# Optimization experiments

Hardware: AMD Instinct MI355X
Metric: run time of the kernel (lower is better)

## Reference

```python
import jax, jax.numpy as jnp
import numpy as np

B, C, H, W = 8, 512, 64, 64
K = 8  # shrink factor: qk channels = C//K, v channels = C//2


def conv1x1(x, w, b):
    # x: [B,C_in,H,W], w: [C_out,C_in], b: [C_out]  (1x1 conv == channel matmul)
    return jnp.einsum('bchw,oc->bohw', x, w) + b[None, :, None, None]


def maxpool2x2(x):
    b, c, h, w = x.shape
    return x.reshape(b, c, h // 2, 2, w // 2, 2).max(axis=(3, 5))


def setup_inputs() -> dict:
    key = jax.random.key(0)
    ks = jax.random.split(key, 9)
    Cqk, Cv = C // K, C // 2
    sc = lambda fan_in: 1.0 / np.sqrt(fan_in)
    return {
        'x': jax.random.normal(ks[0], (B, C, H, W), jnp.float32),
        'Wf': jax.random.normal(ks[1], (Cqk, C), jnp.float32) * sc(C),
        'bf': jnp.zeros((Cqk,), jnp.float32),
        'Wg': jax.random.normal(ks[2], (Cqk, C), jnp.float32) * sc(C),
        'bg': jnp.zeros((Cqk,), jnp.float32),
        'Wh': jax.random.normal(ks[3], (Cv, C), jnp.float32) * sc(C),
        'bh': jnp.zeros((Cv,), jnp.float32),
        'Wv': jax.random.normal(ks[4], (C, Cv), jnp.float32) * sc(Cv),
        'bv': jnp.zeros((C,), jnp.float32),
        'gamma': jnp.float32(0.5),
    }


def reference(x, Wf, bf, Wg, bg, Wh, bh, Wv, bv, gamma):
    b, c, h, w = x.shape
    f = conv1x1(x, Wf, bf).reshape(b, c // K, h * w)          # [B, C/K, HW]
    g = maxpool2x2(conv1x1(x, Wg, bg))                         # [B, C/K, H/2, W/2]
    v = maxpool2x2(conv1x1(x, Wh, bh))                         # [B, C/2, H/2, W/2]
    hwp = (h // 2) * (w // 2)
    g = g.reshape(b, c // K, hwp)
    v = v.reshape(b, c // 2, hwp)
    # s[b, n, m] = sum_c f[b,c,n] g[b,c,m]; softmax over m (no scaling, per SAGAN)
    s = jnp.einsum('bcn,bcm->bnm', f, g)                       # [B, HW, HW']
    beta = jax.nn.softmax(s, axis=-1)
    o = jnp.einsum('bcm,bnm->bcn', v, beta).reshape(b, c // 2, h, w)
    return gamma * conv1x1(o, Wv, bv) + x
```

## Files before the change

kernel.cpp:

```cpp
#include <hip/hip_runtime.h>
#include <cstddef>

typedef __attribute__((ext_vector_type(4))) float f32x4;
typedef __attribute__((ext_vector_type(16))) float f32x16;
typedef __attribute__((ext_vector_type(8))) short bf16x8;

#define MFMA16(A, B, C) __builtin_amdgcn_mfma_f32_16x16x32_bf16(A, B, C, 0, 0, 0)
#define MFMA32(A, B, C) __builtin_amdgcn_mfma_f32_32x32x16_bf16(A, B, C, 0, 0, 0)
#define AS1 __attribute__((address_space(1)))
#define AS3 __attribute__((address_space(3)))

__device__ __forceinline__ unsigned short f2bf(float f) {
  unsigned u = __float_as_uint(f);
  u += 0x7fffu + ((u >> 16) & 1u);
  return (unsigned short)(u >> 16);
}
__device__ __forceinline__ float bf2f(unsigned short s) {
  return __uint_as_float(((unsigned)s) << 16);
}

__device__ __forceinline__ void cvt_split8(float4 a, float4 b, bf16x8* H, bf16x8* L) {
  float v[8] = {a.x, a.y, a.z, a.w, b.x, b.y, b.z, b.w};
  unsigned hh[4], ll[4];
  #pragma unroll
  for (int p = 0; p < 4; ++p) {
    unsigned short h0 = f2bf(v[2 * p]), h1 = f2bf(v[2 * p + 1]);
    hh[p] = (unsigned)h0 | ((unsigned)h1 << 16);
    unsigned short l0 = f2bf(v[2 * p] - bf2f(h0));
    unsigned short l1 = f2bf(v[2 * p + 1] - bf2f(h1));
    ll[p] = (unsigned)l0 | ((unsigned)l1 << 16);
  }
  uint4 uh; uh.x = hh[0]; uh.y = hh[1]; uh.z = hh[2]; uh.w = hh[3];
  uint4 ul; ul.x = ll[0]; ul.y = ll[1]; ul.z = ll[2]; ul.w = ll[3];
  *H = *(bf16x8*)&uh;
  *L = *(bf16x8*)&ul;
}

__device__ __forceinline__ bf16x8 cvt_hi8(float4 a, float4 b) {
  float v[8] = {a.x, a.y, a.z, a.w, b.x, b.y, b.z, b.w};
  unsigned hh[4];
  #pragma unroll
  for (int p = 0; p < 4; ++p)
    hh[p] = (unsigned)f2bf(v[2 * p]) | ((unsigned)f2bf(v[2 * p + 1]) << 16);
  uint4 uh; uh.x = hh[0]; uh.y = hh[1]; uh.z = hh[2]; uh.w = hh[3];
  return *(bf16x8*)&uh;
}


__global__ void prep_k(const float* __restrict__ Wf, const float* __restrict__ Wg,
                       const float* __restrict__ Wh, const float* __restrict__ Wv,
                       unsigned short* __restrict__ wfh, unsigned short* __restrict__ wfl,
                       unsigned short* __restrict__ wgh, unsigned short* __restrict__ wgl,
                       unsigned short* __restrict__ whb, unsigned short* __restrict__ wvb) {
  int i = blockIdx.x * 256 + threadIdx.x;
  if (i < 65536) {
    int ii = i & 32767;
    int j = ii & 7, slot = (ii >> 3) & 63, q = slot & 15, qt2 = slot >> 4;
    int kt = (ii >> 9) & 15, oct = ii >> 13;
    const float* src = (i < 32768) ? Wf : Wg;
    unsigned short* dh = (i < 32768) ? wfh : wgh;
    unsigned short* dl = (i < 32768) ? wfl : wgl;
    float v = src[(oct * 16 + q) * 512 + kt * 32 + qt2 * 8 + j];
    unsigned short h = f2bf(v);
    dh[ii] = h; dl[ii] = f2bf(v - bf2f(h));
  } else if (i < 196608) {
    int ii = i - 65536;
    int j = ii & 7, slot = (ii >> 3) & 63, q = slot & 15, qt2 = slot >> 4;
    int kt = (ii >> 9) & 15, oct = ii >> 13;
    whb[ii] = f2bf(Wh[(oct * 16 + q) * 512 + kt * 32 + qt2 * 8 + j]);
  } else if (i < 327680) {
    int ii = i - 196608;
    int j = ii & 7, slot = (ii >> 3) & 63, q = slot & 15, qt2 = slot >> 4;
    int kt = (ii >> 9) & 7, oct = ii >> 12;
    wvb[ii] = f2bf(Wv[(oct * 16 + q) * 256 + kt * 32 + qt2 * 8 + j]);
  }
}


#define STAGEX(XP, CN) { _Pragma("unroll") \
  for (int c_ = 0; c_ < 4; ++c_) \
    __builtin_amdgcn_global_load_lds( \
      (const AS1 unsigned int*)(xg + (size_t)((CN) * 32 + c_ * 2) * 4096), \
      (AS3 unsigned int*)((XP) + (w * 8 + c_ * 2) * 128), 16, 0, 0); }

#define STAGEW0(WP, CN) { \
  const unsigned short* Wt_ = (w == 0) ? wfh_ : (w == 1) ? wfl_ : (w == 2) ? wgh_ : wgl_; \
  _Pragma("unroll") \
  for (int ot_ = 0; ot_ < 4; ++ot_) \
    __builtin_amdgcn_global_load_lds( \
      (const AS1 unsigned int*)(Wt_ + (((size_t)(ot_ * 16 + (CN))) << 9) + lane * 8), \
      (AS3 unsigned int*)((WP) + (w * 4 + ot_) * 512), 16, 0, 0); }

#define STAGEW1(WP, CN) { _Pragma("unroll") \
  for (int i_ = 0; i_ < 4; ++i_) \
    __builtin_amdgcn_global_load_lds( \
      (const AS1 unsigned int*)(whb_ + (((size_t)((w * 4 + i_) * 16 + (CN))) << 9) + lane * 8), \
      (AS3 unsigned int*)((WP) + (w * 4 + i_) * 512), 16, 0, 0); }

__global__ __launch_bounds__(256, 2)
void conv_all(const float* __restrict__ x,
              const unsigned short* __restrict__ wfh_, const unsigned short* __restrict__ wfl_,
              const unsigned short* __restrict__ wgh_, const unsigned short* __restrict__ wgl_,
              const unsigned short* __restrict__ whb_,
              const float* __restrict__ bf_, const float* __restrict__ bg_,
              const float* __restrict__ bh_,
              unsigned short* __restrict__ fhi, unsigned short* __restrict__ flo,
              unsigned short* __restrict__ ghi, unsigned short* __restrict__ glo,
              unsigned short* __restrict__ vp)
{
  __shared__ __align__(16) char smem[65536];
  float* xs0 = (float*)smem;
  float* xs1 = (float*)(smem + 16384);
  unsigned short* ws0 = (unsigned short*)(smem + 32768);
  unsigned short* ws1 = (unsigned short*)(smem + 49152);
  const int bid = blockIdx.x;
  const int b = bid & 7;
  const int idx = bid >> 3;
  const int role = idx & 1;
  const int hp = idx >> 1;
  const int n0 = hp * 128;
  const int tid = threadIdx.x, w = tid >> 6, lane = tid & 63, q = lane & 15, qt = lane >> 4;
  const float* xg = x + ((size_t)(b * 512 + w * 8 + (lane >> 5)) * 4096) + n0 + (lane & 31) * 4;

  if (role == 0) {
    f32x4 accf[2][4], accg[2][4];
    #pragma unroll
    for (int nt = 0; nt < 2; ++nt)
      #pragma unroll
      for (int ot = 0; ot < 4; ++ot) {
        accf[nt][ot] = (f32x4){0.f, 0.f, 0.f, 0.f};
        accg[nt][ot] = (f32x4){0.f, 0.f, 0.f, 0.f};
      }
    STAGEX(xs0, 0) STAGEW0(ws0, 0)
    __syncthreads();
    for (int cc = 0; cc < 16; ++cc) {
      const float* xsp = (cc & 1) ? xs1 : xs0;
      const unsigned short* wp = (cc & 1) ? ws1 : ws0;
      float* xsn = (cc & 1) ? xs0 : xs1;
      unsigned short* wn = (cc & 1) ? ws0 : ws1;
      if (cc < 15) { STAGEX(xsn, cc + 1) STAGEW0(wn, cc + 1) }
      bf16x8 Ah[2], Al[2];
      #pragma unroll
      for (int nt = 0; nt < 2; ++nt) {
        const int row = w * 32 + nt * 16 + q;
        float xv[8];
        #pragma unroll
        for (int j = 0; j < 8; ++j)
          xv[j] = xsp[(qt * 8 + j) * 128 + row];
        float4 a0; a0.x = xv[0]; a0.y = xv[1]; a0.z = xv[2]; a0.w = xv[3];
        float4 a1; a1.x = xv[4]; a1.y = xv[5]; a1.z = xv[6]; a1.w = xv[7];
        cvt_split8(a0, a1, &Ah[nt], &Al[nt]);
      }
      {
        bf16x8 Bh[4], Bl[4];
        #pragma unroll
        for (int ot = 0; ot < 4; ++ot) {
          Bh[ot] = *(const bf16x8*)&wp[(0 + ot) * 512 + lane * 8];
          Bl[ot] = *(const bf16x8*)&wp[(4 + ot) * 512 + lane * 8];
        }
        #pragma unroll
        for (int nt = 0; nt < 2; ++nt)
          #pragma unroll
          for (int ot = 0; ot < 4; ++ot) {
            accf[nt][ot] = MFMA16(Ah[nt], Bh[ot], accf[nt][ot]);
            accf[nt][ot] = MFMA16(Ah[nt], Bl[ot], accf[nt][ot]);
            accf[nt][ot] = MFMA16(Al[nt], Bh[ot], accf[nt][ot]);
          }
      }
      {
        bf16x8 Bh[4], Bl[4];
        #pragma unroll
        for (int ot = 0; ot < 4; ++ot) {
          Bh[ot] = *(const bf16x8*)&wp[(8 + ot) * 512 + lane * 8];
          Bl[ot] = *(const bf16x8*)&wp[(12 + ot) * 512 + lane * 8];
        }
        #pragma unroll
        for (int nt = 0; nt < 2; ++nt)
          #pragma unroll
          for (int ot = 0; ot < 4; ++ot) {
            accg[nt][ot] = MFMA16(Ah[nt], Bh[ot], accg[nt][ot]);
            accg[nt][ot] = MFMA16(Ah[nt], Bl[ot], accg[nt][ot]);
            accg[nt][ot] = MFMA16(Al[nt], Bh[ot], accg[nt][ot]);
          }
      }
      __syncthreads();
    }
    #pragma unroll
    for (int nt = 0; nt < 2; ++nt)
      #pragma unroll
      for (int ot = 0; ot < 4; ++ot)
        #pragma unroll
        for (int r = 0; r < 4; ++r) {
          float v = accf[nt][ot][r] + bf_[ot * 16 + q];
          unsigned short h = f2bf(v);
          size_t o = (((size_t)(b * 128 + hp * 4 + w) * 4 + ot) * 64 +
                      (q >> 3) * 32 + nt * 16 + qt * 4 + r) * 8 + (q & 7);
          fhi[o] = h;
          flo[o] = f2bf(v - bf2f(h));
        }
    float (*pl)[67] = (float(*)[67])smem;
    #pragma unroll
    for (int nt = 0; nt < 2; ++nt)
      #pragma unroll
      for (int ot = 0; ot < 4; ++ot)
        #pragma unroll
        for (int r = 0; r < 4; ++r)
          pl[w * 32 + nt * 16 + qt * 4 + r][ot * 16 + q] = accg[nt][ot][r];
    __syncthreads();
    const int c = tid & 63;
    #pragma unroll
    for (int it = 0; it < 8; ++it) {
      int wp2 = (tid >> 6) + it * 4;
      float v = fmaxf(fmaxf(pl[2 * wp2][c], pl[2 * wp2 + 1][c]),
                      fmaxf(pl[64 + 2 * wp2][c], pl[65 + 2 * wp2][c])) + bg_[c];
      unsigned short h = f2bf(v);
      size_t o = (((size_t)(b * 32 + hp) * 4 + (c >> 4)) * 64 +
                  ((c >> 3) & 1) * 32 + wp2) * 8 + (c & 7);
      ghi[o] = h;
      glo[o] = f2bf(v - bf2f(h));
    }
  } else {
    f32x4 acc[2][16];
    #pragma unroll
    for (int nt = 0; nt < 2; ++nt)
      #pragma unroll
      for (int ot = 0; ot < 16; ++ot) acc[nt][ot] = (f32x4){0.f, 0.f, 0.f, 0.f};
    STAGEX(xs0, 0) STAGEW1(ws0, 0)
    __syncthreads();
    for (int cc = 0; cc < 16; ++cc) {
      const float* xsp = (cc & 1) ? xs1 : xs0;
      const unsigned short* wp = (cc & 1) ? ws1 : ws0;
      float* xsn = (cc & 1) ? xs0 : xs1;
      unsigned short* wn = (cc & 1) ? ws0 : ws1;
      if (cc < 15) { STAGEX(xsn, cc + 1) STAGEW1(wn, cc + 1) }
      bf16x8 A_[2];
      #pragma unroll
      for (int nt = 0; nt < 2; ++nt) {
        const int row = w * 32 + nt * 16 + q;
        float xv[8];
        #pragma unroll
        for (int j = 0; j < 8; ++j)
          xv[j] = xsp[(qt * 8 + j) * 128 + row];
        float4 a0; a0.x = xv[0]; a0.y = xv[1]; a0.z = xv[2]; a0.w = xv[3];
        float4 a1; a1.x = xv[4]; a1.y = xv[5]; a1.z = xv[6]; a1.w = xv[7];
        A_[nt] = cvt_hi8(a0, a1);
      }
      #pragma unroll
      for (int oh = 0; oh < 2; ++oh) {
        bf16x8 B_[8];
        #pragma unroll
        for (int ot = 0; ot < 8; ++ot)
          B_[ot] = *(const bf16x8*)&wp[(oh * 8 + ot) * 512 + lane * 8];
        #pragma unroll
        for (int nt = 0; nt < 2; ++nt)
          #pragma unroll
          for (int ot = 0; ot < 8; ++ot)
            acc[nt][oh * 8 + ot] = MFMA16(A_[nt], B_[ot], acc[nt][oh * 8 + ot]);
      }
      __syncthreads();
    }
    float (*pl)[67] = (float(*)[67])smem;
    #pragma unroll
    for (int oh = 0; oh < 4; ++oh) {
      if (oh) __syncthreads();
      #pragma unroll
      for (int nt = 0; nt < 2; ++nt)
        #pragma unroll
        for (int ot4 = 0; ot4 < 4; ++ot4)
          #pragma unroll
          for (int r = 0; r < 4; ++r)
            pl[w * 32 + nt * 16 + qt * 4 + r][ot4 * 16 + q] = acc[nt][oh * 4 + ot4][r];
      __syncthreads();
      const int wp2 = tid & 31;
      #pragma unroll
      for (int it = 0; it < 8; ++it) {
        int cc2 = (tid >> 5) + it * 8;
        int cv = oh * 64 + cc2;
        float v = fmaxf(fmaxf(pl[2 * wp2][cc2], pl[2 * wp2 + 1][cc2]),
                        fmaxf(pl[64 + 2 * wp2][cc2], pl[65 + 2 * wp2][cc2])) + bh_[cv];
        size_t o = (((size_t)(b * 16 + (cv >> 4)) * 32 + hp) * 64 +
                    (wp2 >> 3) * 16 + (cv & 15)) * 8 + (wp2 & 7);
        vp[o] = f2bf(v);
      }
    }
  }
}


#define PROW 264

__global__ __launch_bounds__(256, 2)
void attn_mfma(const unsigned short* __restrict__ f_, const unsigned short* __restrict__ fl_,
               const unsigned short* __restrict__ g_, const unsigned short* __restrict__ gl_,
               const unsigned short* __restrict__ vp, unsigned short* __restrict__ oT)
{
  __shared__ __align__(16) unsigned short PB[64 * PROW];
  __shared__ float redm[4][2][32], reds[4][2][32];
  const int b = blockIdx.x & 7, bx = blockIdx.x >> 3;
  const int tid = threadIdx.x, w = tid >> 6, lane = tid & 63;
  const int q32 = lane & 31, hl = lane >> 5;
  const int q16 = lane & 15, qt = lane >> 4;

  bf16x8 Fh[2][4], Fl[2][4];
  #pragma unroll
  for (int qt2 = 0; qt2 < 2; ++qt2) {
    size_t fb = ((size_t)(b * 128 + bx * 2 + qt2) << 11) + lane * 8;
    #pragma unroll
    for (int s = 0; s < 4; ++s) {
      Fh[qt2][s] = *(const bf16x8*)(f_ + fb + (s << 9));
      Fl[qt2][s] = *(const bf16x8*)(fl_ + fb + (s << 9));
    }
  }

  float M0 = -3.0e38f, M1 = -3.0e38f;
  float Mp[4], Sp[4];
  #pragma unroll
  for (int qs = 0; qs < 4; ++qs) { Mp[qs] = -3.0e38f; Sp[qs] = 0.f; }
  f32x4 oacc[4][4];
  #pragma unroll
  for (int c4 = 0; c4 < 4; ++c4)
    #pragma unroll
    for (int qs = 0; qs < 4; ++qs) oacc[c4][qs] = (f32x4){0.f, 0.f, 0.f, 0.f};
  const size_t vroot = ((size_t)(b * 16 + w * 4) * 32) * 512 + lane * 8;

#define VLD(C4, KS) (*(const bf16x8*)(vp + vroot + ((size_t)((C4) * 32 + mc * 8 + (KS)) << 9)))
#define LOADVA(KS) { va0 = VLD(0, KS); va1 = VLD(1, KS); va2 = VLD(2, KS); va3 = VLD(3, KS); }
#define LOADVB(KS) { vb0 = VLD(0, KS); vb1 = VLD(1, KS); vb2 = VLD(2, KS); vb3 = VLD(3, KS); }
#define PVMFMA(KS, V0, V1, V2, V3) { \
  bf16x8 pb0 = *(const bf16x8*)&PB[q16 * PROW + (KS) * 32 + qt * 8]; \
  bf16x8 pb1 = *(const bf16x8*)&PB[(16 + q16) * PROW + (KS) * 32 + qt * 8]; \
  bf16x8 pb2 = *(const bf16x8*)&PB[(32 + q16) * PROW + (KS) * 32 + qt * 8]; \
  bf16x8 pb3 = *(const bf16x8*)&PB[(48 + q16) * PROW + (KS) * 32 + qt * 8]; \
  oacc[0][0] = MFMA16(V0, pb0, oacc[0][0]); oacc[1][0] = MFMA16(V1, pb0, oacc[1][0]); \
  oacc[2][0] = MFMA16(V2, pb0, oacc[2][0]); oacc[3][0] = MFMA16(V3, pb0, oacc[3][0]); \
  oacc[0][1] = MFMA16(V0, pb1, oacc[0][1]); oacc[1][1] = MFMA16(V1, pb1, oacc[1][1]); \
  oacc[2][1] = MFMA16(V2, pb1, oacc[2][1]); oacc[3][1] = MFMA16(V3, pb1, oacc[3][1]); \
  oacc[0][2] = MFMA16(V0, pb2, oacc[0][2]); oacc[1][2] = MFMA16(V1, pb2, oacc[1][2]); \
  oacc[2][2] = MFMA16(V2, pb2, oacc[2][2]); oacc[3][2] = MFMA16(V3, pb2, oacc[3][2]); \
  oacc[0][3] = MFMA16(V0, pb3, oacc[0][3]); oacc[1][3] = MFMA16(V1, pb3, oacc[1][3]); \
  oacc[2][3] = MFMA16(V2, pb3, oacc[2][3]); oacc[3][3] = MFMA16(V3, pb3, oacc[3][3]); }

  #pragma unroll 1
  for (int mc = 0; mc < 4; ++mc) {
    f32x16 sa0t0 = {}, sa0t1 = {}, sa1t0 = {}, sa1t1 = {};
    __builtin_amdgcn_s_setprio(1);
    #pragma unroll
    for (int t = 0; t < 2; ++t) {
      size_t gb = ((size_t)(b * 32 + mc * 8 + w * 2 + t) << 11) + lane * 8;
      bf16x8 Gh[4], Gl[4];
      #pragma unroll
      for (int s = 0; s < 4; ++s) {
        Gh[s] = *(const bf16x8*)(g_ + gb + (s << 9));
        Gl[s] = *(const bf16x8*)(gl_ + gb + (s << 9));
      }
      f32x16* s0 = t ? &sa0t1 : &sa0t0;
      f32x16* s1 = t ? &sa1t1 : &sa1t0;
      #pragma unroll
      for (int s = 0; s < 4; ++s) {
        *s0 = MFMA32(Gh[s], Fh[0][s], *s0);
        *s0 = MFMA32(Gh[s], Fl[0][s], *s0);
        *s0 = MFMA32(Gl[s], Fh[0][s], *s0);
        *s1 = MFMA32(Gh[s], Fh[1][s], *s1);
        *s1 = MFMA32(Gh[s], Fl[1][s], *s1);
        *s1 = MFMA32(Gl[s], Fh[1][s], *s1);
      }
    }
    __builtin_amdgcn_s_setprio(0);

    bf16x8 va0, va1, va2, va3, vb0, vb1, vb2, vb3;
    LOADVA(0)

    float mx0 = -3.0e38f, mx1 = -3.0e38f;
    #pragma unroll
    for (int r = 0; r < 16; ++r) {
      mx0 = fmaxf(mx0, fmaxf(sa0t0[r], sa0t1[r]));
      mx1 = fmaxf(mx1, fmaxf(sa1t0[r], sa1t1[r]));
    }
    mx0 = fmaxf(mx0, __shfl_xor(mx0, 32));
    mx1 = fmaxf(mx1, __shfl_xor(mx1, 32));
    if (lane < 32) { redm[w][0][lane] = mx0; redm[w][1][lane] = mx1; }
    __syncthreads();
    float gmx0 = fmaxf(fmaxf(redm[0][0][q32], redm[1][0][q32]), fmaxf(redm[2][0][q32], redm[3][0][q32]));
    float gmx1 = fmaxf(fmaxf(redm[0][1][q32], redm[1][1][q32]), fmaxf(redm[2][1][q32], redm[3][1][q32]));
    float Mn0 = fmaxf(M0, gmx0), Mn1 = fmaxf(M1, gmx1);
    M0 = Mn0; M1 = Mn1;

    float rfp[4];
    #pragma unroll
    for (int qs = 0; qs < 4; ++qs) {
      int hq = qs >> 1, cq = (qs & 1) * 16 + q16;
      float gm = fmaxf(fmaxf(redm[0][hq][cq], redm[1][hq][cq]),
                       fmaxf(redm[2][hq][cq], redm[3][hq][cq]));
      float Mn = fmaxf(Mp[qs], gm);
      rfp[qs] = __expf(Mp[qs] - Mn);
      Mp[qs] = Mn;
    }

    float cs0 = 0.f, cs1 = 0.f;
    #pragma unroll
    for (int r = 0; r < 16; ++r) {
      float p;
      p = __expf(sa0t0[r] - Mn0); sa0t0[r] = p; cs0 += p;
      p = __expf(sa0t1[r] - Mn0); sa0t1[r] = p; cs0 += p;
      p = __expf(sa1t0[r] - Mn1); sa1t0[r] = p; cs1 += p;
      p = __expf(sa1t1[r] - Mn1); sa1t1[r] = p; cs1 += p;
    }
    cs0 += __shfl_xor(cs0, 32);
    cs1 += __shfl_xor(cs1, 32);
    if (lane < 32) { reds[w][0][lane] = cs0; reds[w][1][lane] = cs1; }

    #pragma unroll
    for (int j = 0; j < 4; ++j) {
      uint2 pk;
      pk.x = (unsigned)f2bf(sa0t0[4*j+0]) | ((unsigned)f2bf(sa0t0[4*j+1]) << 16);
      pk.y = (unsigned)f2bf(sa0t0[4*j+2]) | ((unsigned)f2bf(sa0t0[4*j+3]) << 16);
      *(uint2*)&PB[q32 * PROW + w * 64 + j * 8 + hl * 4] = pk;
      pk.x = (unsigned)f2bf(sa0t1[4*j+0]) | ((unsigned)f2bf(sa0t1[4*j+1]) << 16);
      pk.y = (unsigned)f2bf(sa0t1[4*j+2]) | ((unsigned)f2bf(sa0t1[4*j+3]) << 16);
      *(uint2*)&PB[q32 * PROW + w * 64 + 32 + j * 8 + hl * 4] = pk;
      pk.x = (unsigned)f2bf(sa1t0[4*j+0]) | ((unsigned)f2bf(sa1t0[4*j+1]) << 16);
      pk.y = (unsigned)f2bf(sa1t0[4*j+2]) | ((unsigned)f2bf(sa1t0[4*j+3]) << 16);
      *(uint2*)&PB[(32 + q32) * PROW + w * 64 + j * 8 + hl * 4] = pk;
      pk.x = (unsigned)f2bf(sa1t1[4*j+0]) | ((unsigned)f2bf(sa1t1[4*j+1]) << 16);
      pk.y = (unsigned)f2bf(sa1t1[4*j+2]) | ((unsigned)f2bf(sa1t1[4*j+3]) << 16);
      *(uint2*)&PB[(32 + q32) * PROW + w * 64 + 32 + j * 8 + hl * 4] = pk;
    }
    __syncthreads();

    #pragma unroll
    for (int qs = 0; qs < 4; ++qs) {
      int hq = qs >> 1, cq = (qs & 1) * 16 + q16;
      float ct = reds[0][hq][cq] + reds[1][hq][cq] + reds[2][hq][cq] + reds[3][hq][cq];
      Sp[qs] = (mc == 0) ? ct : Sp[qs] * rfp[qs] + ct;
    }

    if (mc > 0) {
      #pragma unroll
      for (int c4 = 0; c4 < 4; ++c4)
        #pragma unroll
        for (int qs = 0; qs < 4; ++qs) oacc[c4][qs] *= rfp[qs];
    }
    LOADVB(1)
    __builtin_amdgcn_s_setprio(1);
    #pragma unroll
    for (int kp = 0; kp < 4; ++kp) {
      PVMFMA(2 * kp, va0, va1, va2, va3)
      if (2 * kp + 2 < 8) LOADVA(2 * kp + 2)
      PVMFMA(2 * kp + 1, vb0, vb1, vb2, vb3)
      if (2 * kp + 3 < 8) LOADVB(2 * kp + 3)
    }
    __builtin_amdgcn_s_setprio(0);
  }

  __syncthreads();
  float rinv[4];
  #pragma unroll
  for (int qs = 0; qs < 4; ++qs) rinv[qs] = 1.0f / Sp[qs];
  #pragma unroll
  for (int c4 = 0; c4 < 4; ++c4)
    #pragma unroll
    for (int qs = 0; qs < 4; ++qs) {
      uint2 pk;
      pk.x = (unsigned)f2bf(oacc[c4][qs][0] * rinv[qs]) | ((unsigned)f2bf(oacc[c4][qs][1] * rinv[qs]) << 16);
      pk.y = (unsigned)f2bf(oacc[c4][qs][2] * rinv[qs]) | ((unsigned)f2bf(oacc[c4][qs][3] * rinv[qs]) << 16);
      *(uint2*)&PB[(qs * 16 + q16) * PROW + w * 64 + c4 * 16 + qt * 4] = pk;
    }
  __syncthreads();
  const size_t obase = (size_t)(b * 256 + bx * 4) * 4096;
  #pragma unroll
  for (int it = 0; it < 8; ++it) {
    int u = it * 256 + tid;
    int so = u * 8;
    int ntl = so >> 12;
    int rem = so & 4095;
    int ks = rem >> 9;
    int slot = (rem >> 3) & 63;
    int qq = slot & 15, cg = slot >> 4;
    uint4 val = *(const uint4*)&PB[(ntl * 16 + qq) * PROW + ks * 32 + cg * 8];
    *(uint4*)(oT + obase + so) = val;
  }
}


__global__ __launch_bounds__(256)
void conv_final(const unsigned short* __restrict__ A, const unsigned short* __restrict__ W,
                const float* __restrict__ bias, float* __restrict__ out,
                const float* __restrict__ resid, const float* __restrict__ gamma_p)
{
  const int bid = blockIdx.x;
  const int b = bid & 7;
  const int idx = bid >> 3;
  const int n0 = (idx & 31) * 128;
  const int oc0 = (idx >> 5) * 128;
  const int tid = threadIdx.x, w = tid >> 6, lane = tid & 63, q = lane & 15, qt = lane >> 4;

  f32x4 acc[2][8];
  #pragma unroll
  for (int nt = 0; nt < 2; ++nt)
    #pragma unroll
    for (int ot = 0; ot < 8; ++ot) acc[nt][ot] = (f32x4){0.f, 0.f, 0.f, 0.f};

  #pragma unroll
  for (int ks = 0; ks < 8; ++ks) {
    bf16x8 A_[2], B_[8];
    #pragma unroll
    for (int nt = 0; nt < 2; ++nt)
      A_[nt] = *(const bf16x8*)(A + (((size_t)(b * 256 + (n0 >> 4) + w * 2 + nt) * 8 + ks) << 9) + lane * 8);
    #pragma unroll
    for (int ot = 0; ot < 8; ++ot)
      B_[ot] = *(const bf16x8*)(W + (((size_t)((oc0 >> 4) + ot) * 8 + ks) << 9) + lane * 8);
    #pragma unroll
    for (int nt = 0; nt < 2; ++nt)
      #pragma unroll
      for (int ot = 0; ot < 8; ++ot)
        acc[nt][ot] = MFMA16(A_[nt], B_[ot], acc[nt][ot]);
  }

  const float gm = gamma_p[0];
  #pragma unroll
  for (int ot = 0; ot < 8; ++ot) {
    int oc = oc0 + ot * 16 + q;
    float bs = bias[oc];
    #pragma unroll
    for (int nt = 0; nt < 2; ++nt) {
      int n = n0 + w * 32 + nt * 16 + qt * 4;
      size_t o = ((size_t)(b * 512) + oc) * 4096 + n;
      float4 rs = *(const float4*)&resid[o];
      float4 ov;
      ov.x = gm * (acc[nt][ot][0] + bs) + rs.x;
      ov.y = gm * (acc[nt][ot][1] + bs) + rs.y;
      ov.z = gm * (acc[nt][ot][2] + bs) + rs.z;
      ov.w = gm * (acc[nt][ot][3] + bs) + rs.w;
      *(float4*)&out[o] = ov;
    }
  }
}


extern "C" void kernel_launch(void* const* d_in, const int* in_sizes, int n_in,
                              void* d_out, int out_size, void* d_ws, size_t ws_size,
                              hipStream_t stream) {
  const float* x     = (const float*)d_in[0];
  const float* Wf    = (const float*)d_in[1];
  const float* bf    = (const float*)d_in[2];
  const float* Wg    = (const float*)d_in[3];
  const float* bg    = (const float*)d_in[4];
  const float* Wh    = (const float*)d_in[5];
  const float* bh    = (const float*)d_in[6];
  const float* Wv    = (const float*)d_in[7];
  const float* bv    = (const float*)d_in[8];
  const float* gamma = (const float*)d_in[9];
  float* out = (float*)d_out;
  char* w = (char*)d_ws;

  unsigned short* fhi = (unsigned short*)(w);
  unsigned short* flo = (unsigned short*)(w + 4194304);
  unsigned short* ghi = (unsigned short*)(w + 8388608);
  unsigned short* glo = (unsigned short*)(w + 9437184);
  unsigned short* vp  = (unsigned short*)(w + 10485760);
  unsigned short* oT  = (unsigned short*)(w + 14680064);
  unsigned short* wfh = (unsigned short*)(w + 31457280);
  unsigned short* wfl = (unsigned short*)(w + 31522816);
  unsigned short* wgh = (unsigned short*)(w + 31588352);
  unsigned short* wgl = (unsigned short*)(w + 31653888);
  unsigned short* whb = (unsigned short*)(w + 31719424);
  unsigned short* wvb = (unsigned short*)(w + 31981568);

  prep_k<<<1280, 256, 0, stream>>>(Wf, Wg, Wh, Wv, wfh, wfl, wgh, wgl, whb, wvb);

  conv_all<<<512, 256, 0, stream>>>(x, wfh, wfl, wgh, wgl, whb,
                                    bf, bg, bh, fhi, flo, ghi, glo, vp);

  attn_mfma<<<512, 256, 0, stream>>>(fhi, flo, ghi, glo, vp, oT);

  conv_final<<<1024, 256, 0, stream>>>(oT, wvb, bv, out, x, gamma);
}
```

Before: 110.4 us.

## Fuse final 1x1 output convolution and residual into attention kernel epilogue

The attention kernel no longer writes the normalized attention output to a global bf16 buffer for a separate conv_final launch. It keeps the 64-query by 256-channel tile in LDS, laid out in MFMA fragment order, and runs the Wv projection, bias, gamma scaling and residual add directly in its epilogue. This removes one kernel launch and the global write and read of the intermediate oT tensor. In exchange the attention kernel carries a longer epilogue, each block reads the whole Wv weight matrix from global memory, and register pressure may rise under the existing launch bounds.

```diff
diff --git a/kernel.cpp b/kernel.cpp
--- a/kernel.cpp
+++ b/kernel.cpp
@@ -292,7 +292,9 @@
 __global__ __launch_bounds__(256, 2)
 void attn_mfma(const unsigned short* __restrict__ f_, const unsigned short* __restrict__ fl_,
                const unsigned short* __restrict__ g_, const unsigned short* __restrict__ gl_,
-               const unsigned short* __restrict__ vp, unsigned short* __restrict__ oT)
+               const unsigned short* __restrict__ vp, const unsigned short* __restrict__ wv_,
+               const float* __restrict__ bv_, const float* __restrict__ resid,
+               const float* __restrict__ gamma_p, float* __restrict__ out)
 {
   __shared__ __align__(16) unsigned short PB[64 * PROW];
   __shared__ float redm[4][2][32], reds[4][2][32];
@@ -389,9 +391,9 @@
     #pragma unroll
     for (int qs = 0; qs < 4; ++qs) {
       int hq = qs >> 1, cq = (qs & 1) * 16 + q16;
-      float gm = fmaxf(fmaxf(redm[0][hq][cq], redm[1][hq][cq]),
-                       fmaxf(redm[2][hq][cq], redm[3][hq][cq]));
-      float Mn = fmaxf(Mp[qs], gm);
+      float gm2 = fmaxf(fmaxf(redm[0][hq][cq], redm[1][hq][cq]),
+                        fmaxf(redm[2][hq][cq], redm[3][hq][cq]));
+      float Mn = fmaxf(Mp[qs], gm2);
       rfp[qs] = __expf(Mp[qs] - Mn);
       Mp[qs] = Mn;
     }
@@ -463,75 +465,55 @@
       uint2 pk;
       pk.x = (unsigned)f2bf(oacc[c4][qs][0] * rinv[qs]) | ((unsigned)f2bf(oacc[c4][qs][1] * rinv[qs]) << 16);
       pk.y = (unsigned)f2bf(oacc[c4][qs][2] * rinv[qs]) | ((unsigned)f2bf(oacc[c4][qs][3] * rinv[qs]) << 16);
-      *(uint2*)&PB[(qs * 16 + q16) * PROW + w * 64 + c4 * 16 + qt * 4] = pk;
+      int cv = w * 64 + c4 * 16 + qt * 4;
+      int ks = cv >> 5;
+      int sub = (cv & 31) >> 3;
+      int off = (((qs * 8 + ks) * 64 + sub * 16 + q16) << 3) + (qt & 1) * 4;
+      *(uint2*)&PB[off] = pk;
     }
   __syncthreads();
-  const size_t obase = (size_t)(b * 256 + bx * 4) * 4096;
-  #pragma unroll
-  for (int it = 0; it < 8; ++it) {
-    int u = it * 256 + tid;
-    int so = u * 8;
-    int ntl = so >> 12;
-    int rem = so & 4095;
-    int ks = rem >> 9;
-    int slot = (rem >> 3) & 63;
-    int qq = slot & 15, cg = slot >> 4;
-    uint4 val = *(const uint4*)&PB[(ntl * 16 + qq) * PROW + ks * 32 + cg * 8];
-    *(uint4*)(oT + obase + so) = val;
-  }
-}
-
-
-__global__ __launch_bounds__(256)
-void conv_final(const unsigned short* __restrict__ A, const unsigned short* __restrict__ W,
-                const float* __restrict__ bias, float* __restrict__ out,
-                const float* __restrict__ resid, const float* __restrict__ gamma_p)
-{
-  const int bid = blockIdx.x;
-  const int b = bid & 7;
-  const int idx = bid >> 3;
-  const int n0 = (idx & 31) * 128;
-  const int oc0 = (idx >> 5) * 128;
-  const int tid = threadIdx.x, w = tid >> 6, lane = tid & 63, q = lane & 15, qt = lane >> 4;
-
-  f32x4 acc[2][8];
-  #pragma unroll
-  for (int nt = 0; nt < 2; ++nt)
-    #pragma unroll
-    for (int ot = 0; ot < 8; ++ot) acc[nt][ot] = (f32x4){0.f, 0.f, 0.f, 0.f};
-
-  #pragma unroll
-  for (int ks = 0; ks < 8; ++ks) {
-    bf16x8 A_[2], B_[8];
-    #pragma unroll
-    for (int nt = 0; nt < 2; ++nt)
-      A_[nt] = *(const bf16x8*)(A + (((size_t)(b * 256 + (n0 >> 4) + w * 2 + nt) * 8 + ks) << 9) + lane * 8);
-    #pragma unroll
-    for (int ot = 0; ot < 8; ++ot)
-      B_[ot] = *(const bf16x8*)(W + (((size_t)((oc0 >> 4) + ot) * 8 + ks) << 9) + lane * 8);
-    #pragma unroll
-    for (int nt = 0; nt < 2; ++nt)
-      #pragma unroll
-      for (int ot = 0; ot < 8; ++ot)
-        acc[nt][ot] = MFMA16(A_[nt], B_[ot], acc[nt][ot]);
-  }
-
   const float gm = gamma_p[0];
-  #pragma unroll
-  for (int ot = 0; ot < 8; ++ot) {
-    int oc = oc0 + ot * 16 + q;
-    float bs = bias[oc];
-    #pragma unroll
-    for (int nt = 0; nt < 2; ++nt) {
-      int n = n0 + w * 32 + nt * 16 + qt * 4;
-      size_t o = ((size_t)(b * 512) + oc) * 4096 + n;
-      float4 rs = *(const float4*)&resid[o];
-      float4 ov;
-      ov.x = gm * (acc[nt][ot][0] + bs) + rs.x;
-      ov.y = gm * (acc[nt][ot][1] + bs) + rs.y;
-      ov.z = gm * (acc[nt][ot][2] + bs) + rs.z;
-      ov.w = gm * (acc[nt][ot][3] + bs) + rs.w;
-      *(float4*)&out[o] = ov;
+  const int nbase = bx * 64;
+  #pragma unroll
+  for (int oh = 0; oh < 2; ++oh) {
+    f32x4 acc2[4][4];
+    #pragma unroll
+    for (int nt = 0; nt < 4; ++nt)
+      #pragma unroll
+      for (int ot = 0; ot < 4; ++ot) acc2[nt][ot] = (f32x4){0.f, 0.f, 0.f, 0.f};
+    #pragma unroll
+    for (int ks = 0; ks < 8; ++ks) {
+      bf16x8 A_[4], B_[4];
+      #pragma unroll
+      for (int nt = 0; nt < 4; ++nt)
+        A_[nt] = *(const bf16x8*)&PB[((nt * 8 + ks) * 64 + lane) * 8];
+      #pragma unroll
+      for (int ot = 0; ot < 4; ++ot) {
+        int octile = w * 8 + oh * 4 + ot;
+        B_[ot] = *(const bf16x8*)(wv_ + (((size_t)(octile * 8 + ks)) << 9) + lane * 8);
+      }
+      #pragma unroll
+      for (int nt = 0; nt < 4; ++nt)
+        #pragma unroll
+        for (int ot = 0; ot < 4; ++ot)
+          acc2[nt][ot] = MFMA16(A_[nt], B_[ot], acc2[nt][ot]);
+    }
+    #pragma unroll
+    for (int ot = 0; ot < 4; ++ot) {
+      int oc = (w * 8 + oh * 4 + ot) * 16 + q16;
+      float bs = bv_[oc];
+      #pragma unroll
+      for (int nt = 0; nt < 4; ++nt) {
+        int n = nbase + nt * 16 + qt * 4;
+        size_t o = ((size_t)(b * 512) + oc) * 4096 + n;
+        float4 rs = *(const float4*)&resid[o];
+        float4 ov;
+        ov.x = gm * (acc2[nt][ot][0] + bs) + rs.x;
+        ov.y = gm * (acc2[nt][ot][1] + bs) + rs.y;
+        ov.z = gm * (acc2[nt][ot][2] + bs) + rs.z;
+        ov.w = gm * (acc2[nt][ot][3] + bs) + rs.w;
+        *(float4*)&out[o] = ov;
+      }
     }
   }
 }
@@ -558,20 +540,17 @@
   unsigned short* ghi = (unsigned short*)(w + 8388608);
   unsigned short* glo = (unsigned short*)(w + 9437184);
   unsigned short* vp  = (unsigned short*)(w + 10485760);
-  unsigned short* oT  = (unsigned short*)(w + 14680064);
-  unsigned short* wfh = (unsigned short*)(w + 31457280);
-  unsigned short* wfl = (unsigned short*)(w + 31522816);
-  unsigned short* wgh = (unsigned short*)(w + 31588352);
-  unsigned short* wgl = (unsigned short*)(w + 31653888);
-  unsigned short* whb = (unsigned short*)(w + 31719424);
-  unsigned short* wvb = (unsigned short*)(w + 31981568);
+  unsigned short* wfh = (unsigned short*)(w + 14680064);
+  unsigned short* wfl = (unsigned short*)(w + 14745600);
+  unsigned short* wgh = (unsigned short*)(w + 14811136);
+  unsigned short* wgl = (unsigned short*)(w + 14876672);
+  unsigned short* whb = (unsigned short*)(w + 14942208);
+  unsigned short* wvb = (unsigned short*)(w + 15204352);
 
   prep_k<<<1280, 256, 0, stream>>>(Wf, Wg, Wh, Wv, wfh, wfl, wgh, wgl, whb, wvb);
 
   conv_all<<<512, 256, 0, stream>>>(x, wfh, wfl, wgh, wgl, whb,
                                     bf, bg, bh, fhi, flo, ghi, glo, vp);
 
-  attn_mfma<<<512, 256, 0, stream>>>(fhi, flo, ghi, glo, vp, oT);
-
-  conv_final<<<1024, 256, 0, stream>>>(oT, wvb, bv, out, x, gamma);
-}
+  attn_mfma<<<512, 256, 0, stream>>>(fhi, flo, ghi, glo, vp, wvb, bv, x, gamma, out);
+}
```

Result: faster. 100.5 us (-9.0%).
